# Optimization experiments

Measured on AMD Instinct MI355X. Metric: run time of the kernel, lower is better.

## Reference

```python
import jax, jax.numpy as jnp
import numpy as np

N, F_IN, HID, NCLS, E = 100000, 256, 256, 32, 3200000
NHEADS, HDIM, MFEAT = 4, 64, 266  # MFEAT = int(HDIM * ln(HDIM)), performer default
ALPHA, KSTEPS, EPS = 0.1, 10, 1e-4


def setup_inputs() -> dict:
    key = jax.random.key(0)
    ks = jax.random.split(key, 16)
    p = lambda k, sh: (jax.random.normal(k, sh, dtype=jnp.float32) * 0.02)
    return {
        "x": jax.random.normal(ks[0], (N, F_IN), dtype=jnp.float32),
        "edge_index": jax.random.randint(ks[1], (2, E), 0, N, dtype=jnp.int64),
        "lin1_w": p(ks[2], (HID, F_IN)), "lin1_b": p(ks[3], (HID,)),
        "lin2_w": p(ks[4], (NCLS, 2 * HID)), "lin2_b": p(ks[5], (NCLS,)),
        "q_w": p(ks[6], (HID, F_IN)), "q_b": p(ks[7], (HID,)),
        "k_w": p(ks[8], (HID, F_IN)), "k_b": p(ks[9], (HID,)),
        "v_w": p(ks[10], (HID, F_IN)), "v_b": p(ks[11], (HID,)),
        "proj": jax.random.normal(ks[12], (MFEAT, HDIM), dtype=jnp.float32),
    }


def _softmax_kernel(data, proj, is_query):
    # performer_pytorch softmax random-feature map
    d = data.shape[-1]
    m = proj.shape[0]
    dn = d ** -0.25
    ratio = m ** -0.5
    data_dash = jnp.einsum('bhnd,md->bhnm', data * dn, proj)
    diag = 0.5 * (dn ** 2) * jnp.sum(data * data, axis=-1, keepdims=True)  # [b,h,n,1]
    if is_query:
        mx = jax.lax.stop_gradient(jnp.max(data_dash, axis=-1, keepdims=True))
    else:
        mx = jax.lax.stop_gradient(jnp.max(data_dash, axis=(-2, -1), keepdims=True))
    return ratio * (jnp.exp(data_dash - diag - mx) + EPS)


def _fast_attention(q, k, v, proj):
    # non-causal performer linear attention; q,k,v: [b,h,n,d]
    qp = _softmax_kernel(q, proj, True)   # [b,h,n,m]
    kp = _softmax_kernel(k, proj, False)  # [b,h,n,m]
    k_sum = jnp.sum(kp, axis=-2)                                   # [b,h,m]
    d_inv = 1.0 / jnp.einsum('bhnm,bhm->bhn', qp, k_sum)           # [b,h,n]
    context = jnp.einsum('bhnm,bhnd->bhmd', kp, v)                 # [b,h,m,d]
    return jnp.einsum('bhmd,bhnm,bhn->bhnd', context, qp, d_inv)   # [b,h,n,d]


def _appnp(x, edge_index, n):
    # gcn_norm with self-loops, then K iterations of x <- (1-a) A_hat x + a h
    src = jnp.concatenate([edge_index[0], jnp.arange(n, dtype=edge_index.dtype)])
    dst = jnp.concatenate([edge_index[1], jnp.arange(n, dtype=edge_index.dtype)])
    deg = jax.ops.segment_sum(jnp.ones_like(dst, dtype=x.dtype), dst, num_segments=n)
    dis = jnp.where(deg > 0, jax.lax.rsqrt(deg), 0.0)
    w = (dis[src] * dis[dst])[:, None]  # [E+N, 1]
    h = x
    for _ in range(KSTEPS):
        msg = jax.ops.segment_sum(x[src] * w, dst, num_segments=n)
        x = (1.0 - ALPHA) * msg + ALPHA * h
    return x


def reference(x, edge_index, lin1_w, lin1_b, lin2_w, lin2_b,
              q_w, q_b, k_w, k_b, v_w, v_b, proj):
    n = x.shape[0]
    # dropout layers are identity in eval mode
    xu = x[None]  # [1, N, F]
    q = (xu @ q_w.T + q_b).reshape(1, n, NHEADS, HDIM).transpose(0, 2, 1, 3)
    k = (xu @ k_w.T + k_b).reshape(1, n, NHEADS, HDIM).transpose(0, 2, 1, 3)
    v = (xu @ v_w.T + v_b).reshape(1, n, NHEADS, HDIM).transpose(0, 2, 1, 3)
    attn = _fast_attention(q, k, v, proj)                      # [1,h,n,d]
    trans = attn.transpose(0, 2, 1, 3).reshape(n, HID)         # [N, HID]
    gnn1 = x @ lin1_w.T + lin1_b                               # [N, HID]
    cat = jax.nn.elu(jnp.concatenate([gnn1, trans], axis=1))   # [N, 2*HID]
    gnn2 = jax.nn.elu(cat @ lin2_w.T + lin2_b)                 # [N, NCLS]
    final = _appnp(gnn2, edge_index, n)
    return jax.nn.log_softmax(final, axis=1), final
```

## Files before the change

kernel.cpp:

```cpp
#include <hip/hip_runtime.h>
#include <hip/hip_fp16.h>

#define NH 4
#define HD 64
#define MF 266
#define MP 288
#define NB 192
#define NBQ 128
#define DN 0.35355339059327373f
#define RATIO 0.06131393394849658f
#define EPSRF 1e-4f
#define REPS (RATIO*EPSRF)

typedef unsigned short u16;
typedef unsigned int u32;
typedef __attribute__((ext_vector_type(8))) short bf16x8;
typedef __attribute__((ext_vector_type(4))) float f32x4;
#define MFMA16(a,b,c) __builtin_amdgcn_mfma_f32_16x16x32_bf16(a,b,c,0,0,0)

__device__ __forceinline__ float bf2f(u16 u){ return __uint_as_float(((u32)u)<<16); }
__device__ __forceinline__ u16 f2bf(float f){ u32 u = __float_as_uint(f); u += 0x7FFFu + ((u>>16)&1u); return (u16)(u>>16); }
__device__ __forceinline__ u32 pack2bf(float a, float b){ return ((u32)f2bf(b)<<16) | f2bf(a); }
__device__ __forceinline__ float eluf(float x){ return x>0.f ? x : (expf(x)-1.f); }

__global__ void k_cvtw(const float* __restrict__ qw, const float* __restrict__ kw,
                       const float* __restrict__ vw, const float* __restrict__ lw,
                       const float* __restrict__ l2w, const float* __restrict__ proj,
                       u16* __restrict__ Wb, u16* __restrict__ projp, u16* __restrict__ l2wb){
  int i = blockIdx.x*256 + threadIdx.x;
  if (i < 262144){
    int sec = i>>16, r = i&65535;
    const float* s = sec==0?qw : sec==1?kw : sec==2?vw : lw;
    Wb[i] = f2bf(s[r]);
  }
  if (i < MP*64){
    int r = i>>6, c = i&63;
    projp[i] = f2bf(r < MF ? proj[r*64 + c] : 0.f);
  }
  if (i < 32*512) l2wb[i] = f2bf(l2w[i]);
}

__global__ __launch_bounds__(512,6) void k_proj(
    const float* __restrict__ x, const u16* __restrict__ Wb,
    const float* __restrict__ qb, const float* __restrict__ kb,
    const float* __restrict__ vb, const float* __restrict__ lb,
    u16* __restrict__ Q, u16* __restrict__ K, u16* __restrict__ V,
    u16* __restrict__ G1, int n)
{
  __shared__ u32 Xs[64*128];
  const int tid = threadIdx.x;
  const int w = tid>>6, l = tid&63;
  const int wr = w>>2, wc = w&3;
  const int lm = l&15, lk = l>>4;
  const int row0 = blockIdx.x*64;
  #pragma unroll
  for (int q=0;q<8;++q){
    int idx = q*512 + tid;
    int r = idx>>6, c4 = idx&63;
    int rr = row0 + r; if (rr > n-1) rr = n-1;
    float4 v = *(const float4*)(x + (size_t)rr*256 + c4*4);
    int word = (c4*2) ^ ((r&7)<<2);
    *(uint2*)&Xs[r*128 + word] = make_uint2(pack2bf(v.x,v.y), pack2bf(v.z,v.w));
  }
  __syncthreads();
  #pragma unroll 1
  for (int ct=0; ct<8; ++ct){
    const int c0 = ct*128 + wc*32;
    f32x4 acc[2][2] = {};
    #pragma unroll 2
    for (int kt=0; kt<8; ++kt){
      bf16x8 Af[2], Bf[2];
      #pragma unroll
      for (int jj=0;jj<2;jj++)
        Bf[jj] = *(const bf16x8*)(Wb + (size_t)(c0 + jj*16 + lm)*256 + kt*32 + lk*8);
      #pragma unroll
      for (int i=0;i<2;i++){
        const int rl = wr*32 + i*16 + lm;
        Af[i] = *(const bf16x8*)&Xs[rl*128 + ((kt*16 + lk*4) ^ ((rl&7)<<2))];
      }
      #pragma unroll
      for (int i=0;i<2;i++)
        #pragma unroll
        for (int jj=0;jj<2;jj++)
          acc[i][jj] = MFMA16(Af[i], Bf[jj], acc[i][jj]);
    }
    const int sel = c0>>8;
    const float* bp = sel==0?qb : sel==1?kb : sel==2?vb : lb;
    u16* d3 = sel==0?Q : sel==1?K : sel==2?V : G1;
    u32* dst32 = (u32*)d3;
    const bool even = (lm&1)==0;
    #pragma unroll
    for (int jj=0;jj<2;jj++){
      const int cc = (c0&255) + jj*16 + lm;
      const float bias = bp[cc];
      const int ccA = cc & ~1;
      const int hh = ccA>>6, dd = ccA&63;
      #pragma unroll
      for (int i=0;i<2;i++){
        const int rb = row0 + wr*32 + i*16 + lk*4;
        u32 m01 = pack2bf(acc[i][jj][0]+bias, acc[i][jj][1]+bias);
        u32 m23 = pack2bf(acc[i][jj][2]+bias, acc[i][jj][3]+bias);
        u32 oa = __shfl_xor(m01,1);
        u32 ob = __shfl_xor(m23,1);
        u32 wA = even ? ((m01 & 0xffffu) | ((oa & 0xffffu)<<16))
                      : ((ob  & 0xffffu) | ((m23 & 0xffffu)<<16));
        u32 wB = even ? ((m01 >> 16) | (oa & 0xffff0000u))
                      : ((ob  >> 16) | (m23 & 0xffff0000u));
        const int rA = rb + (even ? 0 : 2);
        const int rB = rA + 1;
        if (sel==3){
          if (rA < n) dst32[(size_t)rA*128 + (ccA>>1)] = wA;
          if (rB < n) dst32[(size_t)rB*128 + (ccA>>1)] = wB;
        } else {
          if (rA < n) dst32[(((size_t)hh*n + rA)<<5) + (dd>>1)] = wA;
          if (rB < n) dst32[(((size_t)hh*n + rB)<<5) + (dd>>1)] = wB;
        }
      }
    }
  }
}

__global__ void k_vcs(const u16* __restrict__ Vb, float* __restrict__ vcs, int n){
  const int h = blockIdx.y, tid = threadIdx.x;
  const int d = tid&63, seg = tid>>6;
  float s = 0.f;
  for (int node = blockIdx.x*4 + seg; node < n; node += 256)
    s += bf2f(Vb[(((size_t)h*n + node)<<6) + d]);
  __shared__ float sm[4][64];
  sm[seg][d] = s; __syncthreads();
  if (tid < 64){
    float t2 = sm[0][tid]+sm[1][tid]+sm[2][tid]+sm[3][tid];
    atomicAdd(vcs + h*64 + tid, t2);
  }
}

__global__ __launch_bounds__(256) void k_ctx(
    const u16* __restrict__ Kb, const u16* __restrict__ Vb,
    const u16* __restrict__ projp,
    float* __restrict__ ctxp, float* __restrict__ ksump,
    u32* __restrict__ kmaxg, int n)
{
  __shared__ u32 kpT[288*32];
  __shared__ u16 Vt[64][72];
  __shared__ float redk[4][288];
  const int tid = threadIdx.x;
  const int w = tid>>6, l = tid&63;
  const int bb = blockIdx.x;
  const int h = blockIdx.y;
  const int lm = l&15, lk = l>>4;
  f32x4 cacc[18] = {};
  float ksa[18] = {};
  float mreg = -3.0e38f;
  const int ntile = (n+63)>>6;
  #pragma unroll 1
  for (int t=bb; t<ntile; t+=NB){
    const int n0 = t*64;
    __syncthreads();
    #pragma unroll
    for (int q=0;q<2;q++){
      int e8 = tid + q*256;
      int nn = e8>>3, d0 = (e8&7)*8;
      uint4 rv = make_uint4(0,0,0,0);
      if (n0+nn < n) rv = *(const uint4*)(Vb + (((size_t)h*n + n0+nn)<<6) + d0);
      const u16* pv = (const u16*)&rv;
      #pragma unroll
      for (int s=0;s<8;s++) Vt[d0+s][nn] = pv[s];
    }
    int rr = n0 + w*16 + lm; if (rr > n-1) rr = n-1;
    const u16* Kbase = Kb + (((size_t)h*n + rr)<<6);
    bf16x8 af0 = *(const bf16x8*)(Kbase + lk*8);
    bf16x8 af1 = *(const bf16x8*)(Kbase + 32 + lk*8);
    float dg = 0.f;
    #pragma unroll
    for (int i2=0;i2<8;i2++){
      float a = bf2f(((const u16*)&af0)[i2]);
      float b = bf2f(((const u16*)&af1)[i2]);
      dg += a*a + b*b;
    }
    dg += __shfl_xor(dg,16); dg += __shfl_xor(dg,32);
    dg *= 0.0625f;
    float dgr[4];
    #pragma unroll
    for (int j=0;j<4;j++) dgr[j] = __shfl(dg, lk*4+j, 16);
    #pragma unroll
    for (int mt=0; mt<18; ++mt){
      bf16x8 b0 = *(const bf16x8*)(projp + (size_t)(mt*16+lm)*64 + lk*8);
      bf16x8 b1 = *(const bf16x8*)(projp + (size_t)(mt*16+lm)*64 + 32 + lk*8);
      f32x4 D = {0,0,0,0};
      D = MFMA16(af0, b0, D);
      D = MFMA16(af1, b1, D);
      const int m = mt*16 + lm;
      const bool vm = m < MF;
      float colsum = 0.f;
      u32 pk0 = 0, pk1 = 0;
      #pragma unroll
      for (int j=0;j<4;j++){
        float ddash = DN * D[j];
        float kp = 0.f;
        if (vm && (n0 + w*16 + lk*4 + j) < n){
          kp = RATIO * __expf(ddash - dgr[j]);
          mreg = fmaxf(mreg, ddash);
          colsum += kp;
        }
        if (j<2) pk0 |= ((u32)f2bf(kp)) << (16*j);
        else     pk1 |= ((u32)f2bf(kp)) << (16*(j-2));
      }
      const int wn0 = w*8 + lk*2;
      *(uint2*)&kpT[m*32 + (wn0 ^ ((m&7)<<2))] = make_uint2(pk0, pk1);
      colsum += __shfl_xor(colsum,16); colsum += __shfl_xor(colsum,32);
      ksa[mt] += colsum;
    }
    __syncthreads();
    #pragma unroll
    for (int mt=0; mt<18; ++mt){
      const int m = mt*16 + lm;
      #pragma unroll
      for (int ks=0;ks<2;++ks){
        bf16x8 a = *(const bf16x8*)&kpT[m*32 + ((ks*16 + lk*4) ^ ((m&7)<<2))];
        bf16x8 bv = *(const bf16x8*)&Vt[w*16+lm][ks*32 + lk*8];
        cacc[mt] = MFMA16(a, bv, cacc[mt]);
      }
    }
  }
  float* cp = ctxp + ((size_t)(h*NB + bb))*MP*64;
  #pragma unroll
  for (int mt=0;mt<18;++mt){
    #pragma unroll
    for (int j=0;j<4;j++){
      int m = mt*16 + lk*4 + j;
      cp[(size_t)m*64 + w*16 + lm] = cacc[mt][j];
    }
  }
  if (l < 16){
    #pragma unroll
    for (int mt=0;mt<18;++mt) redk[w][mt*16+lm] = ksa[mt];
  }
  __shared__ float redm[4];
  float mr = mreg;
  #pragma unroll
  for (int s=1;s<64;s<<=1) mr = fmaxf(mr, __shfl_xor(mr, s));
  if (l==0) redm[w] = mr;
  __syncthreads();
  for (int m2=tid; m2<MP; m2+=256){
    float s = redk[0][m2]+redk[1][m2]+redk[2][m2]+redk[3][m2];
    ksump[((size_t)(h*NB+bb))*MP + m2] = s;
  }
  if (tid==0){
    float bm = fmaxf(fmaxf(redm[0],redm[1]), fmaxf(redm[2],redm[3]));
    u32 b = __float_as_uint(bm);
    u32 enc = (b & 0x80000000u) ? ~b : (b | 0x80000000u);
    atomicMax(kmaxg + h, enc);
  }
}

__global__ void k_reduce(const float* __restrict__ ctxp, const float* __restrict__ ksump,
                         const u32* __restrict__ kmaxg, const float* __restrict__ vcs,
                         u16* __restrict__ ctxT, float* __restrict__ ksum, int n)
{
  const int T1 = NH*MP*64;
  int idx = blockIdx.x*256 + threadIdx.x;
  if (idx < T1){
    int h = idx/(MP*64), r = idx - h*MP*64, m = r>>6, d = r&63;
    u32 ee = kmaxg[h]; u32 b = (ee & 0x80000000u) ? (ee ^ 0x80000000u) : ~ee;
    float sc = __expf(-__uint_as_float(b));
    float s = 0.f;
    for (int bb=0; bb<NB; ++bb) s += ctxp[(((size_t)(h*NB+bb))*MP + m)*64 + d];
    float val = (m < MF) ? (sc*s + REPS*vcs[h*64 + d]) : 0.f;
    ctxT[((size_t)h*64 + d)*MP + m] = f2bf(val);
  } else if (idx < T1 + NH*MP){
    int k2 = idx - T1, h = k2/MP, m = k2 - h*MP;
    u32 ee = kmaxg[h]; u32 b = (ee & 0x80000000u) ? (ee ^ 0x80000000u) : ~ee;
    float sc = __expf(-__uint_as_float(b));
    float s = 0.f;
    for (int bb=0; bb<NB; ++bb) s += ksump[((size_t)(h*NB+bb))*MP + m];
    ksum[h*MP + m] = (m < MF) ? (sc*s + REPS*(float)n) : 0.f;
  }
}

__global__ __launch_bounds__(256) void k_qattn(
    const u16* __restrict__ Qb, const u16* __restrict__ projp,
    const u16* __restrict__ ctxT, const float* __restrict__ ksum,
    u16* __restrict__ trans, int n)
{
  __shared__ u32 pj[288*32];
  __shared__ u16 qp_lds[4][16][168];
  const int tid = threadIdx.x;
  const int w = tid>>6, l = tid&63;
  const int h = blockIdx.y;
  const int lm = l&15, lk = l>>4;
  #pragma unroll
  for (int q=0; q<9; ++q){
    int cix = q*256 + tid;
    int row = cix>>3, c4 = (cix&7)*4;
    uint4 v = *(const uint4*)(projp + row*64 + c4*2);
    *(uint4*)&pj[row*32 + (c4 ^ ((row&7)<<2))] = v;
  }
  float ksm[18];
  #pragma unroll
  for (int mt=0;mt<18;++mt) ksm[mt] = ksum[h*MP + mt*16 + lm];
  __syncthreads();
  const int ntile = (n+63)>>6;
  #pragma unroll 1
  for (int t = blockIdx.x; t < ntile; t += NBQ){
    const int nb = t*64 + w*16;
    int rr = nb + lm; if (rr > n-1) rr = n-1;
    const u16* Qbase = Qb + (((size_t)h*n + rr)<<6);
    bf16x8 af0 = *(const bf16x8*)(Qbase + lk*8);
    bf16x8 af1 = *(const bf16x8*)(Qbase + 32 + lk*8);
    float dg = 0.f;
    #pragma unroll
    for (int i2=0;i2<8;i2++){
      float a = bf2f(((const u16*)&af0)[i2]);
      float b = bf2f(((const u16*)&af1)[i2]);
      dg += a*a + b*b;
    }
    dg += __shfl_xor(dg,16); dg += __shfl_xor(dg,32);
    dg *= 0.0625f;
    float dgr[4];
    #pragma unroll
    for (int j=0;j<4;j++) dgr[j] = __shfl(dg, lk*4+j, 16);
    f32x4 D[18];
    #pragma unroll
    for (int mt=0;mt<18;++mt){
      const int m = mt*16 + lm;
      bf16x8 b0 = *(const bf16x8*)&pj[m*32 + ((lk*4) ^ ((m&7)<<2))];
      bf16x8 b1 = *(const bf16x8*)&pj[m*32 + ((16 + lk*4) ^ ((m&7)<<2))];
      f32x4 z = {0,0,0,0};
      z = MFMA16(af0, b0, z);
      z = MFMA16(af1, b1, z);
      D[mt] = z;
    }
    float rmax[4] = {-3.0e38f,-3.0e38f,-3.0e38f,-3.0e38f};
    #pragma unroll
    for (int mt=0;mt<17;++mt){
      const bool vm = (mt<16) || (lm<10);
      #pragma unroll
      for (int j=0;j<4;j++){
        float dd = DN*D[mt][j];
        if (vm) rmax[j] = fmaxf(rmax[j], dd);
      }
    }
    #pragma unroll
    for (int j=0;j<4;j++){
      #pragma unroll
      for (int s=1;s<16;s<<=1) rmax[j] = fmaxf(rmax[j], __shfl_xor(rmax[j], s));
    }
    float den[4] = {0,0,0,0};
    f32x4 o[4] = {{0,0,0,0},{0,0,0,0},{0,0,0,0},{0,0,0,0}};
    #pragma unroll
    for (int mt=0;mt<10;++mt){
      #pragma unroll
      for (int j=0;j<4;j++){
        float qp = RATIO*(__expf(DN*D[mt][j] - dgr[j] - rmax[j]) + EPSRF);
        den[j] += qp * ksm[mt];
        qp_lds[w][lk*4+j][mt*16+lm] = f2bf(qp);
      }
    }
    #pragma unroll
    for (int ks=0;ks<5;++ks){
      bf16x8 av = *(const bf16x8*)&qp_lds[w][lm][ks*32 + lk*8];
      #pragma unroll
      for (int dt=0;dt<4;++dt){
        bf16x8 bv = *(const bf16x8*)(ctxT + (size_t)(h*64 + dt*16 + lm)*MP + ks*32 + lk*8);
        o[dt] = MFMA16(av, bv, o[dt]);
      }
    }
    #pragma unroll
    for (int mt=10;mt<18;++mt){
      #pragma unroll
      for (int j=0;j<4;j++){
        float qp = RATIO*(__expf(DN*D[mt][j] - dgr[j] - rmax[j]) + EPSRF);
        den[j] += qp * ksm[mt];
        qp_lds[w][lk*4+j][(mt-10)*16+lm] = f2bf(qp);
      }
    }
    #pragma unroll
    for (int ks=5;ks<9;++ks){
      bf16x8 av = *(const bf16x8*)&qp_lds[w][lm][(ks-5)*32 + lk*8];
      #pragma unroll
      for (int dt=0;dt<4;++dt){
        bf16x8 bv = *(const bf16x8*)(ctxT + (size_t)(h*64 + dt*16 + lm)*MP + ks*32 + lk*8);
        o[dt] = MFMA16(av, bv, o[dt]);
      }
    }
    #pragma unroll
    for (int j=0;j<4;j++){
      #pragma unroll
      for (int s=1;s<16;s<<=1) den[j] += __shfl_xor(den[j], s);
    }
    #pragma unroll
    for (int j=0;j<4;j++){
      const int node = nb + lk*4 + j;
      if (node < n){
        const float dv = 1.f/den[j];
        #pragma unroll
        for (int dt=0;dt<4;++dt)
          trans[(size_t)node*256 + h*64 + dt*16 + lm] = f2bf(o[dt][j]*dv);
      }
    }
  }
}

__global__ __launch_bounds__(256) void k_gnn2(
    const u16* __restrict__ G1, const u16* __restrict__ trans,
    const u16* __restrict__ l2wb, const float* __restrict__ l2b,
    u16* __restrict__ xb0, int n)
{
  __shared__ u32 cat[64*256];
  const int tid = threadIdx.x;
  const int w = tid>>6, l = tid&63;
  const int lm = l&15, lk = l>>4;
  const int n0 = blockIdx.x*64;
  #pragma unroll
  for (int src=0; src<2; ++src){
    const u16* S = src ? trans : G1;
    #pragma unroll
    for (int q=0;q<8;++q){
      int idx = q*256 + tid;
      int row = idx>>5, v8 = idx&31;
      int rr = n0+row; if (rr > n-1) rr = n-1;
      uint4 raw = *(const uint4*)(S + (size_t)rr*256 + v8*8);
      const u16* p = (const u16*)&raw;
      u32 o2[4];
      #pragma unroll
      for (int t2=0;t2<4;++t2)
        o2[t2] = pack2bf(eluf(bf2f(p[t2*2])), eluf(bf2f(p[t2*2+1])));
      int word = (v8*4 + src*128) ^ ((row&7)<<2);
      *(uint4*)&cat[row*256 + word] = *(uint4*)o2;
    }
  }
  __syncthreads();
  f32x4 acc[2] = {{0,0,0,0},{0,0,0,0}};
  const int rowl = w*16 + lm;
  #pragma unroll 4
  for (int kt=0; kt<16; ++kt){
    bf16x8 a = *(const bf16x8*)&cat[rowl*256 + ((kt*16 + lk*4) ^ ((rowl&7)<<2))];
    #pragma unroll
    for (int jj=0;jj<2;++jj){
      bf16x8 b = *(const bf16x8*)(l2wb + (size_t)(jj*16+lm)*512 + kt*32 + lk*8);
      acc[jj] = MFMA16(a, b, acc[jj]);
    }
  }
  #pragma unroll
  for (int jj=0;jj<2;++jj){
    const int o = jj*16 + lm;
    const float bias = l2b[o];
    #pragma unroll
    for (int jr=0;jr<4;++jr){
      const int node = n0 + w*16 + lk*4 + jr;
      if (node < n)
        xb0[(size_t)node*32 + o] = f2bf(eluf(acc[jj][jr] + bias));
    }
  }
}

__global__ void k_edgemode(const int* __restrict__ ei, int* __restrict__ mode){
  __shared__ int any;
  if (threadIdx.x==0) any = 0;
  __syncthreads();
  if (ei[threadIdx.x*2+1] != 0) any = 1;
  __syncthreads();
  if (threadIdx.x==0) *mode = any;
}
__device__ __forceinline__ int edge_at(const int* ei, int mode, size_t idx){
  if (mode) return ei[idx];
  return (int)((const long long*)ei)[idx];
}

__global__ void k_hist(const int* __restrict__ ei, const int* __restrict__ mode,
                       u32* __restrict__ deg, int e){
  const int md = *mode;
  for (size_t i = (size_t)blockIdx.x*blockDim.x + threadIdx.x; i < (size_t)e; i += (size_t)gridDim.x*blockDim.x)
    atomicAdd(&deg[edge_at(ei, md, (size_t)e + i)], 1u);
}
__global__ void k_dis(const u32* __restrict__ deg, float* __restrict__ dis, int n){
  int i = blockIdx.x*256 + threadIdx.x;
  if (i<n) dis[i] = rsqrtf((float)(deg[i] + 1u));
}
__global__ __launch_bounds__(1024) void k_scan(const u32* __restrict__ deg, u32* __restrict__ rowp, int n){
  __shared__ u32 wsum[16];
  __shared__ u32 carry;
  const int tid = threadIdx.x, lane = tid&63, wv = tid>>6;
  if (tid==0){ carry = 0u; rowp[0] = 0u; }
  __syncthreads();
  for (int base=0; base<n; base+=1024){
    int i = base + tid;
    u32 v = (i<n)? deg[i] : 0u;
    u32 s = v;
    #pragma unroll
    for (int off=1; off<64; off<<=1){
      u32 t = __shfl_up(s, off, 64);
      if (lane >= off) s += t;
    }
    if (lane==63) wsum[wv] = s;
    __syncthreads();
    if (wv==0){
      u32 ws = (lane<16)? wsum[lane] : 0u;
      #pragma unroll
      for (int off=1; off<16; off<<=1){
        u32 t = __shfl_up(ws, off, 64);
        if (lane >= off) ws += t;
      }
      if (lane<16) wsum[lane] = ws;
    }
    __syncthreads();
    u32 pre = carry + (wv ? wsum[wv-1] : 0u);
    if (i<n) rowp[i+1] = pre + s;
    __syncthreads();
    if (tid==0) carry += wsum[15];
    __syncthreads();
  }
}
__global__ void k_copy(const u32* __restrict__ a, u32* __restrict__ b, int n){
  int i = blockIdx.x*256 + threadIdx.x; if (i<n) b[i]=a[i];
}
__global__ void k_fill(const int* __restrict__ ei, const int* __restrict__ mode,
                       const float* __restrict__ dis,
                       u32* __restrict__ cur, uint2* __restrict__ cw, int e){
  const int md = *mode;
  for (size_t i = (size_t)blockIdx.x*blockDim.x + threadIdx.x; i < (size_t)e; i += (size_t)gridDim.x*blockDim.x){
    int s = edge_at(ei, md, i);
    int t = edge_at(ei, md, (size_t)e + i);
    u32 pos = atomicAdd(&cur[t], 1u);
    cw[pos] = make_uint2((u32)s, __float_as_uint(dis[s]*dis[t]));
  }
}

__global__ __launch_bounds__(256) void k_appnp(
    const u16* __restrict__ xin, const u16* __restrict__ hb16,
    u16* __restrict__ xout, const u32* __restrict__ rowp,
    const uint2* __restrict__ cw, const float* __restrict__ dis, int n)
{
  const int g = threadIdx.x>>3, j4 = threadIdx.x&7;
  const int node = blockIdx.x*32 + g;
  if (node >= n) return;
  const uint2* x64 = (const uint2*)xin;
  float d0 = dis[node];
  float dd = d0*d0;
  uint2 xv = x64[((size_t)node<<3) + j4];
  float a0 = dd*bf2f((u16)xv.x), a1 = dd*bf2f((u16)(xv.x>>16));
  float a2 = dd*bf2f((u16)xv.y), a3 = dd*bf2f((u16)(xv.y>>16));
  u32 r0 = rowp[node], r1 = rowp[node+1];
  u32 k = r0;
  for (; k+4 <= r1; k += 4){
    uint2 e0 = cw[k], e1 = cw[k+1], e2 = cw[k+2], e3 = cw[k+3];
    uint2 v0 = x64[((size_t)e0.x<<3)+j4], v1 = x64[((size_t)e1.x<<3)+j4];
    uint2 v2 = x64[((size_t)e2.x<<3)+j4], v3 = x64[((size_t)e3.x<<3)+j4];
    float w0=__uint_as_float(e0.y), w1=__uint_as_float(e1.y);
    float w2=__uint_as_float(e2.y), w3=__uint_as_float(e3.y);
    a0 += w0*bf2f((u16)v0.x) + w1*bf2f((u16)v1.x) + w2*bf2f((u16)v2.x) + w3*bf2f((u16)v3.x);
    a1 += w0*bf2f((u16)(v0.x>>16)) + w1*bf2f((u16)(v1.x>>16)) + w2*bf2f((u16)(v2.x>>16)) + w3*bf2f((u16)(v3.x>>16));
    a2 += w0*bf2f((u16)v0.y) + w1*bf2f((u16)v1.y) + w2*bf2f((u16)v2.y) + w3*bf2f((u16)v3.y);
    a3 += w0*bf2f((u16)(v0.y>>16)) + w1*bf2f((u16)(v1.y>>16)) + w2*bf2f((u16)(v2.y>>16)) + w3*bf2f((u16)(v3.y>>16));
  }
  for (; k < r1; ++k){
    uint2 e = cw[k];
    uint2 v = x64[((size_t)e.x<<3)+j4];
    float wgt = __uint_as_float(e.y);
    a0 += wgt*bf2f((u16)v.x);
    a1 += wgt*bf2f((u16)(v.x>>16));
    a2 += wgt*bf2f((u16)v.y);
    a3 += wgt*bf2f((u16)(v.y>>16));
  }
  uint2 hv = ((const uint2*)hb16)[((size_t)node<<3) + j4];
  uint2 o;
  o.x = pack2bf(0.9f*a0 + 0.1f*bf2f((u16)hv.x), 0.9f*a1 + 0.1f*bf2f((u16)(hv.x>>16)));
  o.y = pack2bf(0.9f*a2 + 0.1f*bf2f((u16)hv.y), 0.9f*a3 + 0.1f*bf2f((u16)(hv.y>>16)));
  ((uint2*)xout)[((size_t)node<<3) + j4] = o;
}

__global__ __launch_bounds__(256) void k_appnp_lsm(
    const u16* __restrict__ xin, const u16* __restrict__ hb16,
    float* __restrict__ out, const u32* __restrict__ rowp,
    const uint2* __restrict__ cw, const float* __restrict__ dis, int n)
{
  const int g = threadIdx.x>>3, j4 = threadIdx.x&7;
  const int node = blockIdx.x*32 + g;
  if (node >= n) return;
  const uint2* x64 = (const uint2*)xin;
  float d0 = dis[node];
  float dd = d0*d0;
  uint2 xv = x64[((size_t)node<<3) + j4];
  float a0 = dd*bf2f((u16)xv.x), a1 = dd*bf2f((u16)(xv.x>>16));
  float a2 = dd*bf2f((u16)xv.y), a3 = dd*bf2f((u16)(xv.y>>16));
  u32 r0 = rowp[node], r1 = rowp[node+1];
  u32 k = r0;
  for (; k+4 <= r1; k += 4){
    uint2 e0 = cw[k], e1 = cw[k+1], e2 = cw[k+2], e3 = cw[k+3];
    uint2 v0 = x64[((size_t)e0.x<<3)+j4], v1 = x64[((size_t)e1.x<<3)+j4];
    uint2 v2 = x64[((size_t)e2.x<<3)+j4], v3 = x64[((size_t)e3.x<<3)+j4];
    float w0=__uint_as_float(e0.y), w1=__uint_as_float(e1.y);
    float w2=__uint_as_float(e2.y), w3=__uint_as_float(e3.y);
    a0 += w0*bf2f((u16)v0.x) + w1*bf2f((u16)v1.x) + w2*bf2f((u16)v2.x) + w3*bf2f((u16)v3.x);
    a1 += w0*bf2f((u16)(v0.x>>16)) + w1*bf2f((u16)(v1.x>>16)) + w2*bf2f((u16)(v2.x>>16)) + w3*bf2f((u16)(v3.x>>16));
    a2 += w0*bf2f((u16)v0.y) + w1*bf2f((u16)v1.y) + w2*bf2f((u16)v2.y) + w3*bf2f((u16)v3.y);
    a3 += w0*bf2f((u16)(v0.y>>16)) + w1*bf2f((u16)(v1.y>>16)) + w2*bf2f((u16)(v2.y>>16)) + w3*bf2f((u16)(v3.y>>16));
  }
  for (; k < r1; ++k){
    uint2 e = cw[k];
    uint2 v = x64[((size_t)e.x<<3)+j4];
    float wgt = __uint_as_float(e.y);
    a0 += wgt*bf2f((u16)v.x);
    a1 += wgt*bf2f((u16)(v.x>>16));
    a2 += wgt*bf2f((u16)v.y);
    a3 += wgt*bf2f((u16)(v.y>>16));
  }
  uint2 hv = ((const uint2*)hb16)[((size_t)node<<3) + j4];
  float v0 = 0.9f*a0 + 0.1f*bf2f((u16)hv.x);
  float v1 = 0.9f*a1 + 0.1f*bf2f((u16)(hv.x>>16));
  float v2 = 0.9f*a2 + 0.1f*bf2f((u16)hv.y);
  float v3 = 0.9f*a3 + 0.1f*bf2f((u16)(hv.y>>16));
  float m = fmaxf(fmaxf(v0,v1), fmaxf(v2,v3));
  #pragma unroll
  for (int o2=1;o2<8;o2<<=1) m = fmaxf(m, __shfl_xor(m, o2, 8));
  float s = __expf(v0-m)+__expf(v1-m)+__expf(v2-m)+__expf(v3-m);
  #pragma unroll
  for (int o2=1;o2<8;o2<<=1) s += __shfl_xor(s, o2, 8);
  float ls = m + logf(s);
  float4 lsv = make_float4(v0-ls, v1-ls, v2-ls, v3-ls);
  *(float4*)(out + (size_t)node*32 + j4*4) = lsv;
  float4 raw = make_float4(v0, v1, v2, v3);
  *(float4*)(out + (size_t)n*32 + (size_t)node*32 + j4*4) = raw;
}

extern "C" void kernel_launch(void* const* d_in, const int* in_sizes, int n_in,
                              void* d_out, int out_size, void* d_ws, size_t ws_size,
                              hipStream_t stream)
{
  const float* x   = (const float*)d_in[0];
  const int*   ei  = (const int*)  d_in[1];
  const float* l1w = (const float*)d_in[2];
  const float* l1b = (const float*)d_in[3];
  const float* l2w = (const float*)d_in[4];
  const float* l2b = (const float*)d_in[5];
  const float* qw  = (const float*)d_in[6];
  const float* qb  = (const float*)d_in[7];
  const float* kw  = (const float*)d_in[8];
  const float* kb  = (const float*)d_in[9];
  const float* vw  = (const float*)d_in[10];
  const float* vb  = (const float*)d_in[11];
  const float* proj= (const float*)d_in[12];
  const int n = in_sizes[0] / 256;
  const int e = in_sizes[1] / 2;

  char* ws = (char*)d_ws;
  auto au = [](size_t v){ return (v + 255) & ~(size_t)255; };
  const size_t bQ = (size_t)n * 512;
  const size_t oQ = 0;
  const size_t oK = au(oQ + bQ);
  const size_t oV = au(oK + bQ);
  const size_t oG1 = au(oV + bQ);
  const size_t oCtxp = au(oG1 + bQ);
  const size_t bCtxp = (size_t)NH*NB*MP*64*4;
  const size_t oKsump = au(oCtxp + bCtxp);
  const size_t bKsump = (size_t)NH*NB*MP*4;
  const size_t oCtxT = au(oKsump + bKsump);
  const size_t oKsum = au(oCtxT + (size_t)NH*64*MP*2);
  const size_t oKmax = au(oKsum + (size_t)NH*MP*4);
  const size_t oVcs  = oKmax + 256;
  const size_t oMode = oVcs + 1024;
  const size_t oL2wb = au(oMode + 256);
  const size_t oWb   = au(oL2wb + 32768);
  const size_t oProjp= au(oWb + (size_t)1024*256*2);
  const size_t oTrans = oK;
  const size_t oG2 = oQ;
  const size_t oXb0 = au(oG2 + (size_t)n*32*4);
  const size_t oXbA = au(oXb0 + (size_t)n*32*2);
  const size_t oXbB = au(oXbA + (size_t)n*32*2);
  const size_t oDeg = au(oXbB + (size_t)n*32*2);
  const size_t oDis = au(oDeg + (size_t)n*4);
  const size_t oRowp= au(oDis + (size_t)n*4);
  const size_t oCur = au(oRowp + (size_t)(n+1)*4);
  const size_t oCw  = oV;
  (void)ws_size; (void)n_in; (void)out_size;

  u16* Q  = (u16*)(ws + oQ);
  u16* Kb = (u16*)(ws + oK);
  u16* Vb = (u16*)(ws + oV);
  u16* G1 = (u16*)(ws + oG1);
  float* ctxp = (float*)(ws + oCtxp);
  float* ksump= (float*)(ws + oKsump);
  u16*  ctxT  = (u16*)(ws + oCtxT);
  float* ksum = (float*)(ws + oKsum);
  u32*  kmax  = (u32*)(ws + oKmax);
  float* Vcs  = (float*)(ws + oVcs);
  int*  mode  = (int*)(ws + oMode);
  u16*  l2wb  = (u16*)(ws + oL2wb);
  u16*  Wb    = (u16*)(ws + oWb);
  u16*  projp = (u16*)(ws + oProjp);
  u16* trans  = (u16*)(ws + oTrans);
  u16* xb0    = (u16*)(ws + oXb0);
  u16* xbA    = (u16*)(ws + oXbA);
  u16* xbB    = (u16*)(ws + oXbB);
  u32* deg    = (u32*)(ws + oDeg);
  float* dis  = (float*)(ws + oDis);
  u32* rowp   = (u32*)(ws + oRowp);
  u32* cur    = (u32*)(ws + oCur);
  uint2* cw   = (uint2*)(ws + oCw);

  k_cvtw<<<1024,256,0,stream>>>(qw,kw,vw,l1w,l2w,proj,Wb,projp,l2wb);
  k_proj<<<(n+63)/64,512,0,stream>>>(x,Wb,qb,kb,vb,l1b,Q,Kb,Vb,G1,n);
  hipMemsetAsync(ws + oKmax, 0, 16, stream);
  hipMemsetAsync(ws + oVcs, 0, 1024, stream);
  k_vcs<<<dim3(64,4),256,0,stream>>>(Vb,Vcs,n);
  k_ctx<<<dim3(NB,NH),256,0,stream>>>(Kb,Vb,projp,ctxp,ksump,kmax,n);
  {
    int tot = NH*MP*64 + NH*MP;
    k_reduce<<<(tot+255)/256,256,0,stream>>>(ctxp,ksump,kmax,Vcs,ctxT,ksum,n);
  }
  k_qattn<<<dim3(NBQ,4),256,0,stream>>>(Q,projp,ctxT,ksum,trans,n);
  k_gnn2<<<(n+63)/64,256,0,stream>>>(G1,trans,l2wb,l2b,xb0,n);
  k_edgemode<<<1,256,0,stream>>>(ei,mode);
  hipMemsetAsync(ws + oDeg, 0, (size_t)n*4, stream);
  k_hist<<<2048,256,0,stream>>>(ei,mode,deg,e);
  k_dis<<<(n+255)/256,256,0,stream>>>(deg,dis,n);
  k_scan<<<1,1024,0,stream>>>(deg,rowp,n);
  k_copy<<<(n+255)/256,256,0,stream>>>(rowp,cur,n);
  k_fill<<<2048,256,0,stream>>>(ei,mode,dis,cur,cw,e);
  const u16* curx = xb0;
  u16* bufs[2] = {xbA, xbB};
  for (int it=0; it<9; ++it){
    u16* nxt = bufs[it&1];
    k_appnp<<<(n+31)/32,256,0,stream>>>(curx,xb0,nxt,rowp,cw,dis,n);
    curx = nxt;
  }
  k_appnp_lsm<<<(n+31)/32,256,0,stream>>>(curx,xb0,(float*)d_out,rowp,cw,dis,n);
}
```

Before: 1.576 ms.

## Enlarge projection GEMM row tile and parallelize CSR degree scan

The projection GEMM now covers 128 rows per block instead of 64, so each wave computes a 64x32 tile and every loaded weight fragment is reused across twice as many rows. This needs twice the shared memory and more accumulator registers, and the occupancy hint drops to 4. Separately, the single-block serial prefix scan over node degrees becomes a three-stage scan (per-block sums, a scan of those sums, then per-block local scans), which removes a long single-workgroup loop at the cost of two extra launches.

```diff
diff --git a/kernel.cpp b/kernel.cpp
--- a/kernel.cpp
+++ b/kernel.cpp
@@ -40,21 +40,21 @@
   if (i < 32*512) l2wb[i] = f2bf(l2w[i]);
 }
 
-__global__ __launch_bounds__(512,6) void k_proj(
+__global__ __launch_bounds__(512,4) void k_proj(
     const float* __restrict__ x, const u16* __restrict__ Wb,
     const float* __restrict__ qb, const float* __restrict__ kb,
     const float* __restrict__ vb, const float* __restrict__ lb,
     u16* __restrict__ Q, u16* __restrict__ K, u16* __restrict__ V,
     u16* __restrict__ G1, int n)
 {
-  __shared__ u32 Xs[64*128];
+  __shared__ u32 Xs[128*128];
   const int tid = threadIdx.x;
   const int w = tid>>6, l = tid&63;
   const int wr = w>>2, wc = w&3;
   const int lm = l&15, lk = l>>4;
-  const int row0 = blockIdx.x*64;
-  #pragma unroll
-  for (int q=0;q<8;++q){
+  const int row0 = blockIdx.x*128;
+  #pragma unroll 4
+  for (int q=0;q<16;++q){
     int idx = q*512 + tid;
     int r = idx>>6, c4 = idx&63;
     int rr = row0 + r; if (rr > n-1) rr = n-1;
@@ -66,20 +66,20 @@
   #pragma unroll 1
   for (int ct=0; ct<8; ++ct){
     const int c0 = ct*128 + wc*32;
-    f32x4 acc[2][2] = {};
+    f32x4 acc[4][2] = {};
     #pragma unroll 2
     for (int kt=0; kt<8; ++kt){
-      bf16x8 Af[2], Bf[2];
+      bf16x8 Af[4], Bf[2];
       #pragma unroll
       for (int jj=0;jj<2;jj++)
         Bf[jj] = *(const bf16x8*)(Wb + (size_t)(c0 + jj*16 + lm)*256 + kt*32 + lk*8);
       #pragma unroll
-      for (int i=0;i<2;i++){
-        const int rl = wr*32 + i*16 + lm;
+      for (int i=0;i<4;i++){
+        const int rl = wr*64 + i*16 + lm;
         Af[i] = *(const bf16x8*)&Xs[rl*128 + ((kt*16 + lk*4) ^ ((rl&7)<<2))];
       }
       #pragma unroll
-      for (int i=0;i<2;i++)
+      for (int i=0;i<4;i++)
         #pragma unroll
         for (int jj=0;jj<2;jj++)
           acc[i][jj] = MFMA16(Af[i], Bf[jj], acc[i][jj]);
@@ -96,8 +96,8 @@
       const int ccA = cc & ~1;
       const int hh = ccA>>6, dd = ccA&63;
       #pragma unroll
-      for (int i=0;i<2;i++){
-        const int rb = row0 + wr*32 + i*16 + lk*4;
+      for (int i=0;i<4;i++){
+        const int rb = row0 + wr*64 + i*16 + lk*4;
         u32 m01 = pack2bf(acc[i][jj][0]+bias, acc[i][jj][1]+bias);
         u32 m23 = pack2bf(acc[i][jj][2]+bias, acc[i][jj][3]+bias);
         u32 oa = __shfl_xor(m01,1);
@@ -477,15 +477,33 @@
   int i = blockIdx.x*256 + threadIdx.x;
   if (i<n) dis[i] = rsqrtf((float)(deg[i] + 1u));
 }
-__global__ __launch_bounds__(1024) void k_scan(const u32* __restrict__ deg, u32* __restrict__ rowp, int n){
+__global__ __launch_bounds__(256) void k_bsum(const u32* __restrict__ deg,
+                                              u32* __restrict__ bsum, int n){
+  __shared__ u32 red[4];
+  const int tid = threadIdx.x, lane = tid&63, wv = tid>>6;
+  const int base = blockIdx.x*1024;
+  u32 s = 0;
+  #pragma unroll
+  for (int q=0;q<4;++q){
+    int i = base + q*256 + tid;
+    if (i<n) s += deg[i];
+  }
+  #pragma unroll
+  for (int off=1; off<64; off<<=1) s += __shfl_xor(s, off, 64);
+  if (lane==0) red[wv] = s;
+  __syncthreads();
+  if (tid==0) bsum[blockIdx.x] = red[0]+red[1]+red[2]+red[3];
+}
+__global__ __launch_bounds__(1024) void k_bscan(u32* __restrict__ bsum,
+                                                u32* __restrict__ rowp, int nblk){
   __shared__ u32 wsum[16];
   __shared__ u32 carry;
   const int tid = threadIdx.x, lane = tid&63, wv = tid>>6;
   if (tid==0){ carry = 0u; rowp[0] = 0u; }
   __syncthreads();
-  for (int base=0; base<n; base+=1024){
+  for (int base=0; base<nblk; base+=1024){
     int i = base + tid;
-    u32 v = (i<n)? deg[i] : 0u;
+    u32 v = (i<nblk)? bsum[i] : 0u;
     u32 s = v;
     #pragma unroll
     for (int off=1; off<64; off<<=1){
@@ -504,12 +522,38 @@
       if (lane<16) wsum[lane] = ws;
     }
     __syncthreads();
-    u32 pre = carry + (wv ? wsum[wv-1] : 0u);
-    if (i<n) rowp[i+1] = pre + s;
+    if (i<nblk) bsum[i] = carry + (wv ? wsum[wv-1] : 0u) + s - v;
     __syncthreads();
     if (tid==0) carry += wsum[15];
     __syncthreads();
   }
+}
+__global__ __launch_bounds__(1024) void k_scan2(const u32* __restrict__ deg,
+                                                const u32* __restrict__ bsum,
+                                                u32* __restrict__ rowp, int n){
+  __shared__ u32 wsum[16];
+  const int tid = threadIdx.x, lane = tid&63, wv = tid>>6;
+  const int i = blockIdx.x*1024 + tid;
+  u32 v = (i<n)? deg[i] : 0u;
+  u32 s = v;
+  #pragma unroll
+  for (int off=1; off<64; off<<=1){
+    u32 t = __shfl_up(s, off, 64);
+    if (lane >= off) s += t;
+  }
+  if (lane==63) wsum[wv] = s;
+  __syncthreads();
+  if (wv==0){
+    u32 ws = (lane<16)? wsum[lane] : 0u;
+    #pragma unroll
+    for (int off=1; off<16; off<<=1){
+      u32 t = __shfl_up(ws, off, 64);
+      if (lane >= off) ws += t;
+    }
+    if (lane<16) wsum[lane] = ws;
+  }
+  __syncthreads();
+  if (i<n) rowp[i+1] = bsum[blockIdx.x] + (wv ? wsum[wv-1] : 0u) + s;
 }
 __global__ void k_copy(const u32* __restrict__ a, u32* __restrict__ b, int n){
   int i = blockIdx.x*256 + threadIdx.x; if (i<n) b[i]=a[i];
@@ -671,6 +715,7 @@
   const size_t oDis = au(oDeg + (size_t)n*4);
   const size_t oRowp= au(oDis + (size_t)n*4);
   const size_t oCur = au(oRowp + (size_t)(n+1)*4);
+  const size_t oBsum= au(oCur + (size_t)(n+1)*4);
   const size_t oCw  = oV;
   (void)ws_size; (void)n_in; (void)out_size;
 
@@ -696,10 +741,11 @@
   float* dis  = (float*)(ws + oDis);
   u32* rowp   = (u32*)(ws + oRowp);
   u32* cur    = (u32*)(ws + oCur);
+  u32* bsum   = (u32*)(ws + oBsum);
   uint2* cw   = (uint2*)(ws + oCw);
 
   k_cvtw<<<1024,256,0,stream>>>(qw,kw,vw,l1w,l2w,proj,Wb,projp,l2wb);
-  k_proj<<<(n+63)/64,512,0,stream>>>(x,Wb,qb,kb,vb,l1b,Q,Kb,Vb,G1,n);
+  k_proj<<<(n+127)/128,512,0,stream>>>(x,Wb,qb,kb,vb,l1b,Q,Kb,Vb,G1,n);
   hipMemsetAsync(ws + oKmax, 0, 16, stream);
   hipMemsetAsync(ws + oVcs, 0, 1024, stream);
   k_vcs<<<dim3(64,4),256,0,stream>>>(Vb,Vcs,n);
@@ -714,7 +760,12 @@
   hipMemsetAsync(ws + oDeg, 0, (size_t)n*4, stream);
   k_hist<<<2048,256,0,stream>>>(ei,mode,deg,e);
   k_dis<<<(n+255)/256,256,0,stream>>>(deg,dis,n);
-  k_scan<<<1,1024,0,stream>>>(deg,rowp,n);
+  {
+    const int nblk = (n+1023)/1024;
+    k_bsum<<<nblk,256,0,stream>>>(deg,bsum,n);
+    k_bscan<<<1,1024,0,stream>>>(bsum,rowp,nblk);
+    k_scan2<<<nblk,1024,0,stream>>>(deg,bsum,rowp,n);
+  }
   k_copy<<<(n+255)/256,256,0,stream>>>(rowp,cur,n);
   k_fill<<<2048,256,0,stream>>>(ei,mode,dis,cur,cw,e);
   const u16* curx = xb0;
```

Result: faster. 1.404 ms (-10.9%).
